# Optimization experiments

Hardware: AMD Instinct MI355X
Metric: run time of the kernel (lower is better)

Reference implementation:

```python
import jax, jax.numpy as jnp
import numpy as np


def ste_round(x):
    # straight-through rounding (identity gradient), as used in brevitas fake-quant
    return x + jax.lax.stop_gradient(jnp.round(x) - x)


def quant_weight(w, bits):
    # symmetric per-tensor int quantization: scale = max|w| / (2^(b-1)-1)
    qmax = 2.0 ** (bits - 1) - 1.0
    s = jnp.max(jnp.abs(w)) / qmax
    return jnp.clip(ste_round(w / s), -qmax, qmax) * s


def quant_relu(x, scale, bits):
    # unsigned act quant (QuantReLU): clip to [0, scale], round to 2^b-1 levels
    n = 2.0 ** bits - 1.0
    step = scale / n
    return ste_round(jnp.clip(x, 0.0, scale) / step) * step


def conv2d(x, w, b, pad):
    # NCHW 'same' conv, stride 1
    y = jax.lax.conv_general_dilated(
        x, w, window_strides=(1, 1),
        padding=[(pad, pad), (pad, pad)],
        dimension_numbers=('NCHW', 'OIHW', 'NCHW'))
    return y + b[None, :, None, None]


def setup_inputs() -> dict:
    key = jax.random.key(0)
    ks = jax.random.split(key, 8)
    B, H, W = 8, 512, 512
    x = jax.random.uniform(ks[0], (B, 1, H, W), dtype=jnp.float32)
    # xavier-ish init scales: gain / sqrt(fan_in + fan_out per kernel elem)
    w1 = jax.random.normal(ks[1], (64, 1, 9, 9), dtype=jnp.float32) * 0.12
    b1 = jax.random.normal(ks[2], (64,), dtype=jnp.float32) * 0.01
    w2 = jax.random.normal(ks[3], (32, 64, 5, 5), dtype=jnp.float32) * 0.03
    b2 = jax.random.normal(ks[4], (32,), dtype=jnp.float32) * 0.01
    w3 = jax.random.normal(ks[5], (1, 32, 5, 5), dtype=jnp.float32) * 0.05
    b3 = jax.random.normal(ks[6], (1,), dtype=jnp.float32) * 0.01
    # activation quant scales (learned params in brevitas; fixed here)
    s1 = jnp.ones((1,), dtype=jnp.float32) * 4.0
    s2 = jnp.ones((1,), dtype=jnp.float32) * 4.0
    s3 = jnp.ones((1,), dtype=jnp.float32) * 2.0
    return {"x": x, "w1": w1, "b1": b1, "w2": w2, "b2": b2,
            "w3": w3, "b3": b3, "s1": s1, "s2": s2, "s3": s3}


def reference(x, w1, b1, w2, b2, w3, b3, s1, s2, s3):
    NBK, NBA, NLACT = 8, 8, 8
    # conv1: 1->64, k=9, pad=4, int8 weights; quant-ReLU (nba bits)
    h = conv2d(x, quant_weight(w1, NBK), b1, pad=4)
    h = quant_relu(h, s1[0], NBA)
    # conv2: 64->32, k=5, pad=2
    h = conv2d(h, quant_weight(w2, NBK), b2, pad=2)
    h = quant_relu(h, s2[0], NBA)
    # conv3: 32->1, k=5, pad=2, last-layer weight bits = nlact = 8
    h = conv2d(h, quant_weight(w3, NLACT), b3, pad=2)
    h = quant_relu(h, s3[0], NLACT)
    return h
```

## Files before the change

kernel.cpp:

```cpp
#include <hip/hip_runtime.h>
#include <cmath>

#define HH 512
#define WW 512
#define BB 8
#define WP (WW + 4)
#define HP (HH + 4)

#define PROWS 520
#define PCOLS 528
#define PT ((size_t)BB * PROWS * PCOLS)

typedef int v4i __attribute__((ext_vector_type(4)));
typedef float v4f __attribute__((ext_vector_type(4)));
typedef _Float16 v8h __attribute__((ext_vector_type(8)));

#if defined(__has_builtin)
#if __has_builtin(__builtin_amdgcn_sdot4)
#define DOT4(a, b, c) __builtin_amdgcn_sdot4((a), (b), (c), false)
#endif
#endif
#ifndef DOT4
static __device__ __forceinline__ int dot4_fb(int a, int b, int c) {
  c += ((a << 24) >> 24) * ((b << 24) >> 24);
  c += ((a << 16) >> 24) * ((b << 16) >> 24);
  c += ((a << 8) >> 24) * ((b << 8) >> 24);
  c += (a >> 24) * (b >> 24);
  return c;
}
#define DOT4(a, b, c) dot4_fb((a), (b), (c))
#endif

static constexpr size_t SCALES_OFF = 0;
static constexpr size_t CORRF_OFF  = 64;
static constexpr size_t FS3_OFF    = 512;
static constexpr size_t QW1_OFF    = 1024;
static constexpr size_t W1FRAG_OFF = 24576;
static constexpr size_t W2S_OFF    = 65536;
static constexpr size_t W3P_OFF    = 131072;
static constexpr size_t H1_OFF     = (size_t)1 << 20;
static constexpr size_t H1_SZ      = (size_t)BB * HP * WP * 64;
static constexpr size_t H2_OFF     = H1_OFF + H1_SZ;
static constexpr size_t H2_SZ      = (size_t)BB * HP * WP * 32;
static constexpr size_t WS_NEED    = H2_OFF + H2_SZ;

__global__ void quant_weights_k(const float* __restrict__ w1,
                                const float* __restrict__ w2,
                                const float* __restrict__ w3,
                                float* __restrict__ scales,
                                float* __restrict__ qw1,
                                signed char* __restrict__ w2s,
                                signed char* __restrict__ w3p) {
  const int t = blockIdx.x;
  const float* src = (t == 0) ? w1 : (t == 1) ? w2 : w3;
  const int n = (t == 0) ? 64 * 81 : (t == 1) ? 32 * 64 * 25 : 32 * 25;
  __shared__ float red[256];
  float m = 0.0f;
  for (int i = threadIdx.x; i < n; i += 256) m = fmaxf(m, fabsf(src[i]));
  red[threadIdx.x] = m;
  __syncthreads();
  for (int s = 128; s > 0; s >>= 1) {
    if ((int)threadIdx.x < s) red[threadIdx.x] = fmaxf(red[threadIdx.x], red[threadIdx.x + s]);
    __syncthreads();
  }
  const float scale = red[0] / 127.0f;
  if (threadIdx.x == 0) scales[t] = scale;
  for (int i = threadIdx.x; i < n; i += 256) {
    float q = rintf(src[i] / scale);
    q = fminf(fmaxf(q, -127.0f), 127.0f);
    if (t == 0) {
      qw1[i] = q;
    } else if (t == 1) {
      const int oc = i / 1600;
      const int r = i - oc * 1600;
      const int ic = r / 25, tap = r - ic * 25;
      w2s[(((tap * 4 + (ic >> 4)) * 32) + oc) * 16 + (ic & 15)] = (signed char)(int)q;
    } else {
      const int ic = i / 25, tap = i - ic * 25;
      w3p[tap * 32 + ic] = (signed char)(int)q;
    }
  }
}

__global__ void prep_k(const signed char* __restrict__ w2s,
                       const signed char* __restrict__ w3p,
                       const float* __restrict__ qw1,
                       int* __restrict__ corrf, int* __restrict__ fs3,
                       unsigned short* __restrict__ w1frag) {
  const int tid = threadIdx.x;
  __shared__ int red3[32];
  {
    const int oc = tid >> 3, part = tid & 7;
    const unsigned int* wd = (const unsigned int*)w2s;
    int s = 0;
    for (int chunk = part; chunk < 100; chunk += 8) {
      const int tap = chunk >> 2, kb = chunk & 3;
      const int base = tap * 512 + kb * 128 + oc * 4;
      #pragma unroll
      for (int j = 0; j < 4; ++j) s = DOT4((int)wd[base + j], 0x01010101, s);
    }
    s += __shfl_xor(s, 1);
    s += __shfl_xor(s, 2);
    s += __shfl_xor(s, 4);
    if (part == 0) corrf[oc] = s;
  }
  if (tid < 32) {
    int s = 0;
    if (tid < 25) {
      const unsigned int* wd = (const unsigned int*)w3p;
      #pragma unroll
      for (int j = 0; j < 8; ++j) s = DOT4((int)wd[tid * 8 + j], 0x01010101, s);
    }
    red3[tid] = s;
  }
  __syncthreads();
  if (tid == 0) {
    int s = 0;
    #pragma unroll
    for (int j = 0; j < 32; ++j) s += red3[j];
    fs3[0] = s;
  }
  for (int i = tid; i < 18432; i += 256) {
    const int e = i & 7, lidx = (i >> 3) & 63, nn = (i >> 9) & 3, j = i >> 11;
    const int t = j * 32 + (lidx >> 4) * 8 + e;
    const int term = (t >= 144) ? 1 : 0;
    const int rem = t - term * 144;
    const int ky = rem >> 4, kx = rem & 15;
    const int oc = nn * 16 + (lidx & 15);
    float v = 0.0f;
    if (kx < 9) v = qw1[oc * 81 + ky * 9 + kx];
    if (term) v *= (1.0f / 4096.0f);
    const _Float16 hv = (_Float16)v;
    w1frag[i] = __builtin_bit_cast(unsigned short, hv);
  }
}

__global__ __launch_bounds__(256) void prep_x_k(const float* __restrict__ x,
                                                unsigned short* __restrict__ planes) {
  const size_t i = (size_t)blockIdx.x * 256 + threadIdx.x;
  if (i >= PT) return;
  const int col = (int)(i % PCOLS);
  const size_t t = i / PCOLS;
  const int row = (int)(t % PROWS);
  const int b = (int)(t / PROWS);
  const float* xb = x + (size_t)b * HH * WW;
  const int xr = row - 4;
  float v0 = 0.0f, v1 = 0.0f;
  if (xr >= 0 && xr < HH) {
    const int c0 = col - 4, c1 = col - 3;
    if (c0 >= 0 && c0 < WW) v0 = xb[(size_t)xr * WW + c0];
    if (c1 >= 0 && c1 < WW) v1 = xb[(size_t)xr * WW + c1];
  }
  const _Float16 h0 = (_Float16)v0;
  const _Float16 l0 = (_Float16)((v0 - (float)h0) * 4096.0f);
  const _Float16 h1 = (_Float16)v1;
  const _Float16 l1 = (_Float16)((v1 - (float)h1) * 4096.0f);
  planes[i]          = __builtin_bit_cast(unsigned short, h0);
  planes[PT + i]     = __builtin_bit_cast(unsigned short, l0);
  planes[2 * PT + i] = __builtin_bit_cast(unsigned short, h1);
  planes[3 * PT + i] = __builtin_bit_cast(unsigned short, l1);
}

__global__ void fill_k(unsigned char* __restrict__ h1p, unsigned char* __restrict__ h2p) {
  const int idx = blockIdx.x * 256 + threadIdx.x;
  const uint4 v = make_uint4(0x80808080u, 0x80808080u, 0x80808080u, 0x80808080u);
  if (idx < 66048) {
    const int q = idx & 3; const int u = idx >> 2;
    const int pxi = u % WP; const int rr = u / WP;
    const int bb = rr >> 2, sel = rr & 3;
    const int row = (sel < 2) ? sel : 512 + sel;
    *(uint4*)(h1p + (((size_t)bb * HP + row) * WP + pxi) * 64 + q * 16) = v;
  } else if (idx < 131584) {
    const int e = idx - 66048; const int q = e & 3; int u = e >> 2;
    const int c = u & 3; u >>= 2;
    const int row = 2 + (u & 511); const int bb = u >> 9;
    const int col = (c < 2) ? c : 512 + c;
    *(uint4*)(h1p + (((size_t)bb * HP + row) * WP + col) * 64 + q * 16) = v;
  } else if (idx < 164608) {
    const int e = idx - 131584; const int q = e & 1; const int u = e >> 1;
    const int pxi = u % WP; const int rr = u / WP;
    const int bb = rr >> 2, sel = rr & 3;
    const int row = (sel < 2) ? sel : 512 + sel;
    *(uint4*)(h2p + (((size_t)bb * HP + row) * WP + pxi) * 32 + q * 16) = v;
  } else {
    const int e = idx - 164608; const int q = e & 1; int u = e >> 1;
    const int c = u & 3; u >>= 2;
    const int row = 2 + (u & 511); const int bb = u >> 9;
    const int col = (c < 2) ? c : 512 + c;
    *(uint4*)(h2p + (((size_t)bb * HP + row) * WP + col) * 32 + q * 16) = v;
  }
}

__global__ __launch_bounds__(512) void conv1_k(
    const unsigned short* __restrict__ planes,
    const unsigned short* __restrict__ w1frag,
    const float* __restrict__ b1,
    const float* __restrict__ scales,
    const float* __restrict__ s1,
    unsigned char* __restrict__ h1p) {
  __shared__ alignas(16) unsigned short wf[18432];
  for (int i = threadIdx.x; i < 2304; i += 512)
    ((int4*)wf)[i] = ((const int4*)w1frag)[i];
  __syncthreads();

  const int y = blockIdx.x & (HH - 1);
  const int b = blockIdx.x >> 9;
  const int l = threadIdx.x & 63;
  const int wv = threadIdx.x >> 6;
  const int pxw = wv * 64;
  const int r = l & 15, kb = l >> 4;

  const unsigned short* pb = planes + (size_t)(r & 1) * (2 * PT)
                           + ((size_t)b * PROWS + y) * PCOLS + (pxw + (r & ~1));
  int offs[9];
  #pragma unroll
  for (int j = 0; j < 9; ++j) {
    const int t0 = j * 32 + kb * 8;
    const int term = (t0 >= 144) ? 1 : 0;
    const int rem = t0 - term * 144;
    offs[j] = term * (int)PT + (rem >> 4) * PCOLS + (rem & 8);
  }

  v4f acc[4][4];
  #pragma unroll
  for (int p = 0; p < 4; ++p)
    #pragma unroll
    for (int o = 0; o < 4; ++o) acc[p][o] = (v4f){0.f, 0.f, 0.f, 0.f};

  #pragma unroll
  for (int j = 0; j < 9; ++j) {
    v8h av[4];
    #pragma unroll
    for (int p = 0; p < 4; ++p) {
      const void* ap = __builtin_assume_aligned((const void*)(pb + offs[j] + p * 16), 4);
      uint4 tv;
      __builtin_memcpy(&tv, ap, 16);
      av[p] = __builtin_bit_cast(v8h, tv);
    }
    #pragma unroll
    for (int o = 0; o < 4; ++o) {
      const v8h bw = *(const v8h*)(wf + ((size_t)(j * 4 + o) * 64 + l) * 8);
      #pragma unroll
      for (int p = 0; p < 4; ++p)
        acc[p][o] = __builtin_amdgcn_mfma_f32_16x16x32_f16(bw, av[p], acc[p][o], 0, 0, 0);
    }
  }

  const float ws1 = scales[0];
  const float sc = s1[0], step = sc / 255.0f;
  unsigned int* ob = (unsigned int*)(h1p
      + (((size_t)b * HP + y + 2) * WP + 2 + pxw + r) * 64 + kb * 4);
  #pragma unroll
  for (int o = 0; o < 4; ++o) {
    const v4f bv = *(const v4f*)(b1 + o * 16 + kb * 4);
    #pragma unroll
    for (int p = 0; p < 4; ++p) {
      unsigned int dw = 0;
      #pragma unroll
      for (int reg = 0; reg < 4; ++reg) {
        const float h = acc[p][o][reg] * ws1 + bv[reg];
        const float c = fminf(fmaxf(h, 0.0f), sc);
        int qi = (int)rintf(c / step);
        qi = qi < 0 ? 0 : (qi > 255 ? 255 : qi);
        dw |= (unsigned int)(qi ^ 0x80) << (8 * reg);
      }
      ob[p * 256 + o * 4] = dw;
    }
  }
}

__global__ __launch_bounds__(256) void conv2_k(
    const unsigned char* __restrict__ h1p,
    const signed char* __restrict__ w2g,
    const int* __restrict__ corrf,
    const float* __restrict__ b2,
    const float* __restrict__ scales,
    const float* __restrict__ s1, const float* __restrict__ s2,
    unsigned char* __restrict__ h2p) {
  const int l = threadIdx.x & 63;
  const int wv = threadIdx.x >> 6;
  const int r = l & 15, kb = l >> 4;
  const int y = blockIdx.y * 4;
  const int b = blockIdx.z;
  const int xw = blockIdx.x * 64 + wv * 16;

  v4i acc[4][2];
  #pragma unroll
  for (int t = 0; t < 4; ++t)
    #pragma unroll
    for (int n = 0; n < 2; ++n) acc[t][n] = (v4i){0, 0, 0, 0};

  const size_t rstride = (size_t)WP * 64;
  const unsigned char* abase = h1p + (((size_t)b * HP + y) * WP + xw + r) * 64 + kb * 16;
  const signed char* wl = w2g + kb * 512 + r * 16;

  v4i a_cur[8], a_nxt[8];
  #pragma unroll
  for (int j = 0; j < 8; ++j) a_cur[j] = *(const v4i*)(abase + j * rstride);

  #pragma unroll
  for (int kx = 0; kx < 5; ++kx) {
    if (kx < 4) {
      #pragma unroll
      for (int j = 0; j < 8; ++j)
        a_nxt[j] = *(const v4i*)(abase + (kx + 1) * 64 + j * rstride);
    }
    #pragma unroll
    for (int ky = 0; ky < 5; ++ky) {
      const signed char* wt = wl + (ky * 5 + kx) * 2048;
      const v4i bf0 = *(const v4i*)(wt);
      const v4i bf1 = *(const v4i*)(wt + 256);
      #pragma unroll
      for (int t = 0; t < 4; ++t) {
        acc[t][0] = __builtin_amdgcn_mfma_i32_16x16x64_i8(bf0, a_cur[ky + t], acc[t][0], 0, 0, 0);
        acc[t][1] = __builtin_amdgcn_mfma_i32_16x16x64_i8(bf1, a_cur[ky + t], acc[t][1], 0, 0, 0);
      }
    }
    if (kx < 4) {
      #pragma unroll
      for (int j = 0; j < 8; ++j) a_cur[j] = a_nxt[j];
    }
  }

  const float step1 = s1[0] / 255.0f;
  const float sc2 = s2[0], step2 = sc2 / 255.0f;
  const float asc = step1 * scales[1];
  #pragma unroll
  for (int n = 0; n < 2; ++n) {
    const v4f bv = *(const v4f*)(b2 + n * 16 + kb * 4);
    const v4i cv = *(const v4i*)(corrf + n * 16 + kb * 4);
    #pragma unroll
    for (int t = 0; t < 4; ++t) {
      unsigned int* ob = (unsigned int*)(h2p
          + (((size_t)b * HP + y + t + 2) * WP + xw + 2 + r) * 32 + n * 16 + kb * 4);
      unsigned int dw = 0;
      #pragma unroll
      for (int reg = 0; reg < 4; ++reg) {
        const float v = (float)(acc[t][n][reg] + cv[reg] * 128) * asc + bv[reg];
        const float c = fminf(fmaxf(v, 0.0f), sc2);
        int qi = (int)rintf(c / step2);
        qi = qi < 0 ? 0 : (qi > 255 ? 255 : qi);
        dw |= (unsigned int)(qi ^ 0x80) << (8 * reg);
      }
      *ob = dw;
    }
  }
}

__global__ __launch_bounds__(256) void conv3_k(
    const unsigned char* __restrict__ h2p,
    const signed char* __restrict__ w3p,
    const int* __restrict__ fs3,
    const float* __restrict__ b3,
    const float* __restrict__ scales,
    const float* __restrict__ s2, const float* __restrict__ s3,
    float* __restrict__ out) {
  const int p  = blockIdx.x * 256 + threadIdx.x;
  const int px = p & (WW - 1);
  const int py = (p >> 9) & (HH - 1);
  const int bz = p >> 18;

  const int* wq = (const int*)w3p;
  const unsigned char* base = h2p + (((size_t)bz * HP + py) * WP + px) * 32;

  int acc = 0;
  #pragma unroll
  for (int ky = 0; ky < 5; ++ky) {
    const v4i* rp = (const v4i*)(base + (size_t)ky * WP * 32);
    v4i c[10];
    #pragma unroll
    for (int g = 0; g < 10; ++g) c[g] = rp[g];
    const int* wrow = wq + ky * 40;
    #pragma unroll
    for (int kx = 0; kx < 5; ++kx) {
      #pragma unroll
      for (int g = 0; g < 8; ++g) {
        const int idx = kx * 8 + g;
        acc = DOT4(c[idx >> 2][idx & 3], wrow[idx], acc);
      }
    }
  }

  const int tot = acc + fs3[0] * 128;
  const float step2 = s2[0] / 255.0f;
  const float sc3 = s3[0], step3 = sc3 / 255.0f;
  const float y = (float)tot * (step2 * scales[2]) + b3[0];
  const float c = fminf(fmaxf(y, 0.0f), sc3);
  float q = rintf(c / step3);
  q = fminf(fmaxf(q, 0.0f), 255.0f);
  out[p] = q * step3;
}

extern "C" void kernel_launch(void* const* d_in, const int* in_sizes, int n_in,
                              void* d_out, int out_size, void* d_ws, size_t ws_size,
                              hipStream_t stream) {
  const float* x  = (const float*)d_in[0];
  const float* w1 = (const float*)d_in[1];
  const float* b1 = (const float*)d_in[2];
  const float* w2 = (const float*)d_in[3];
  const float* b2 = (const float*)d_in[4];
  const float* w3 = (const float*)d_in[5];
  const float* b3 = (const float*)d_in[6];
  const float* s1 = (const float*)d_in[7];
  const float* s2 = (const float*)d_in[8];
  const float* s3 = (const float*)d_in[9];

  if (ws_size < WS_NEED) return;

  char* ws = (char*)d_ws;
  float*          scales  = (float*)(ws + SCALES_OFF);
  int*            corrf   = (int*)(ws + CORRF_OFF);
  int*            fs3     = (int*)(ws + FS3_OFF);
  float*          qw1     = (float*)(ws + QW1_OFF);
  unsigned short* w1frag  = (unsigned short*)(ws + W1FRAG_OFF);
  signed char*    w2s     = (signed char*)(ws + W2S_OFF);
  signed char*    w3p     = (signed char*)(ws + W3P_OFF);
  unsigned char*  h1p     = (unsigned char*)(ws + H1_OFF);
  unsigned char*  h2p     = (unsigned char*)(ws + H2_OFF);
  unsigned short* planes  = (unsigned short*)(ws + H2_OFF);

  quant_weights_k<<<3, 256, 0, stream>>>(w1, w2, w3, scales, qw1, w2s, w3p);
  prep_k<<<1, 256, 0, stream>>>(w2s, w3p, qw1, corrf, fs3, w1frag);
  prep_x_k<<<(int)(PT / 256), 256, 0, stream>>>(x, planes);

  conv1_k<<<BB * HH, 512, 0, stream>>>(planes, w1frag, b1, scales, s1, h1p);
  fill_k<<<771, 256, 0, stream>>>(h1p, h2p);

  dim3 g2(8, 128, BB);
  conv2_k<<<g2, 256, 0, stream>>>(h1p, w2s, corrf, b2, scales, s1, s2, h2p);

  const int npix = BB * HH * WW;
  conv3_k<<<npix / 256, 256, 0, stream>>>(h2p, w3p, fs3, b3, scales, s2, s3, (float*)d_out);
}
```

Measured before the change: 487.0 us.

## Switch conv2 to 32x32x32 int8 MFMA with LDS-staged weights

Rewrites conv2 to use the 32x32x32 int8 MFMA, so each wave covers 32 pixels by all 32 output channels instead of issuing paired 16x16x64 ops. The full 50KB quantized weight tensor is copied into shared memory per block and read from there, and the weight layout in the quantization and correction-sum kernels is changed to match the new fragment order. The grid now gives each wave its own 4-row strip. This should improve MFMA efficiency and cut global weight reads, at the cost of a per-block weight copy and high LDS use that may limit occupancy. The old register prefetch of the next kx activations is also dropped.

Result: faster. 440.7 us (-9.5%).

```diff
diff --git a/kernel.cpp b/kernel.cpp
--- a/kernel.cpp
+++ b/kernel.cpp
@@ -12,6 +12,7 @@
 #define PT ((size_t)BB * PROWS * PCOLS)
 
 typedef int v4i __attribute__((ext_vector_type(4)));
+typedef int v16i __attribute__((ext_vector_type(16)));
 typedef float v4f __attribute__((ext_vector_type(4)));
 typedef _Float16 v8h __attribute__((ext_vector_type(8)));
 
@@ -74,7 +75,9 @@
       const int oc = i / 1600;
       const int r = i - oc * 1600;
       const int ic = r / 25, tap = r - ic * 25;
-      w2s[(((tap * 4 + (ic >> 4)) * 32) + oc) * 16 + (ic & 15)] = (signed char)(int)q;
+      const int addr = (tap * 2 + (ic >> 5)) * 1024 + ((ic >> 4) & 1) * 512
+                     + oc * 16 + (ic & 15);
+      w2s[addr] = (signed char)(int)q;
     } else {
       const int ic = i / 25, tap = i - ic * 25;
       w3p[tap * 32 + ic] = (signed char)(int)q;
@@ -94,8 +97,7 @@
     const unsigned int* wd = (const unsigned int*)w2s;
     int s = 0;
     for (int chunk = part; chunk < 100; chunk += 8) {
-      const int tap = chunk >> 2, kb = chunk & 3;
-      const int base = tap * 512 + kb * 128 + oc * 4;
+      const int base = chunk * 128 + oc * 4;
       #pragma unroll
       for (int j = 0; j < 4; ++j) s = DOT4((int)wd[base + j], 0x01010101, s);
     }
@@ -271,54 +273,56 @@
 
 __global__ __launch_bounds__(256) void conv2_k(
     const unsigned char* __restrict__ h1p,
-    const signed char* __restrict__ w2g,
+    const int4* __restrict__ w2s,
     const int* __restrict__ corrf,
     const float* __restrict__ b2,
     const float* __restrict__ scales,
     const float* __restrict__ s1, const float* __restrict__ s2,
     unsigned char* __restrict__ h2p) {
+  __shared__ alignas(16) signed char wlds[51200];
+  __shared__ alignas(16) int clds[32];
+  {
+    int4* dst = (int4*)wlds;
+    for (int i = threadIdx.x; i < 3200; i += 256) dst[i] = w2s[i];
+    if (threadIdx.x < 32) clds[threadIdx.x] = corrf[threadIdx.x];
+  }
+  __syncthreads();
+
   const int l = threadIdx.x & 63;
   const int wv = threadIdx.x >> 6;
-  const int r = l & 15, kb = l >> 4;
-  const int y = blockIdx.y * 4;
+  const int pl = l & 31;
+  const int hi = l >> 5;
+  const int y = blockIdx.y * 16 + wv * 4;
   const int b = blockIdx.z;
-  const int xw = blockIdx.x * 64 + wv * 16;
-
-  v4i acc[4][2];
+  const int xw = blockIdx.x * 32;
+
+  v16i acc[4];
   #pragma unroll
   for (int t = 0; t < 4; ++t)
     #pragma unroll
-    for (int n = 0; n < 2; ++n) acc[t][n] = (v4i){0, 0, 0, 0};
+    for (int e = 0; e < 16; ++e) acc[t][e] = 0;
 
   const size_t rstride = (size_t)WP * 64;
-  const unsigned char* abase = h1p + (((size_t)b * HP + y) * WP + xw + r) * 64 + kb * 16;
-  const signed char* wl = w2g + kb * 512 + r * 16;
-
-  v4i a_cur[8], a_nxt[8];
-  #pragma unroll
-  for (int j = 0; j < 8; ++j) a_cur[j] = *(const v4i*)(abase + j * rstride);
+  const unsigned char* abase = h1p + (((size_t)b * HP + y) * WP + xw + pl) * 64 + hi * 16;
+  const signed char* wbase = wlds + l * 16;
 
   #pragma unroll
   for (int kx = 0; kx < 5; ++kx) {
-    if (kx < 4) {
-      #pragma unroll
-      for (int j = 0; j < 8; ++j)
-        a_nxt[j] = *(const v4i*)(abase + (kx + 1) * 64 + j * rstride);
+    v4i a[8][2];
+    #pragma unroll
+    for (int row = 0; row < 8; ++row) {
+      a[row][0] = *(const v4i*)(abase + kx * 64 + row * rstride);
+      a[row][1] = *(const v4i*)(abase + kx * 64 + row * rstride + 32);
     }
     #pragma unroll
     for (int ky = 0; ky < 5; ++ky) {
-      const signed char* wt = wl + (ky * 5 + kx) * 2048;
-      const v4i bf0 = *(const v4i*)(wt);
-      const v4i bf1 = *(const v4i*)(wt + 256);
-      #pragma unroll
-      for (int t = 0; t < 4; ++t) {
-        acc[t][0] = __builtin_amdgcn_mfma_i32_16x16x64_i8(bf0, a_cur[ky + t], acc[t][0], 0, 0, 0);
-        acc[t][1] = __builtin_amdgcn_mfma_i32_16x16x64_i8(bf1, a_cur[ky + t], acc[t][1], 0, 0, 0);
+      #pragma unroll
+      for (int h = 0; h < 2; ++h) {
+        const v4i wfr = *(const v4i*)(wbase + ((ky * 5 + kx) * 2 + h) * 1024);
+        #pragma unroll
+        for (int t = 0; t < 4; ++t)
+          acc[t] = __builtin_amdgcn_mfma_i32_32x32x32_i8(wfr, a[ky + t][h], acc[t], 0, 0, 0);
       }
-    }
-    if (kx < 4) {
-      #pragma unroll
-      for (int j = 0; j < 8; ++j) a_cur[j] = a_nxt[j];
     }
   }
 
@@ -326,23 +330,23 @@
   const float sc2 = s2[0], step2 = sc2 / 255.0f;
   const float asc = step1 * scales[1];
   #pragma unroll
-  for (int n = 0; n < 2; ++n) {
-    const v4f bv = *(const v4f*)(b2 + n * 16 + kb * 4);
-    const v4i cv = *(const v4i*)(corrf + n * 16 + kb * 4);
-    #pragma unroll
-    for (int t = 0; t < 4; ++t) {
-      unsigned int* ob = (unsigned int*)(h2p
-          + (((size_t)b * HP + y + t + 2) * WP + xw + 2 + r) * 32 + n * 16 + kb * 4);
+  for (int t = 0; t < 4; ++t) {
+    unsigned char* ob = h2p + (((size_t)b * HP + y + t + 2) * WP + xw + 2 + pl) * 32 + hi * 4;
+    #pragma unroll
+    for (int g = 0; g < 4; ++g) {
+      const int ocb = g * 8 + hi * 4;
+      const v4f bv = *(const v4f*)(b2 + ocb);
+      const v4i cv = *(const v4i*)(clds + ocb);
       unsigned int dw = 0;
       #pragma unroll
-      for (int reg = 0; reg < 4; ++reg) {
-        const float v = (float)(acc[t][n][reg] + cv[reg] * 128) * asc + bv[reg];
+      for (int q = 0; q < 4; ++q) {
+        const float v = (float)(acc[t][g * 4 + q] + cv[q] * 128) * asc + bv[q];
         const float c = fminf(fmaxf(v, 0.0f), sc2);
         int qi = (int)rintf(c / step2);
         qi = qi < 0 ? 0 : (qi > 255 ? 255 : qi);
-        dw |= (unsigned int)(qi ^ 0x80) << (8 * reg);
+        dw |= (unsigned int)(qi ^ 0x80) << (8 * q);
       }
-      *ob = dw;
+      *(unsigned int*)(ob + g * 8) = dw;
     }
   }
 }
@@ -426,8 +430,8 @@
   conv1_k<<<BB * HH, 512, 0, stream>>>(planes, w1frag, b1, scales, s1, h1p);
   fill_k<<<771, 256, 0, stream>>>(h1p, h2p);
 
-  dim3 g2(8, 128, BB);
-  conv2_k<<<g2, 256, 0, stream>>>(h1p, w2s, corrf, b2, scales, s1, s2, h2p);
+  dim3 g2(16, 32, BB);
+  conv2_k<<<g2, 256, 0, stream>>>(h1p, (const int4*)w2s, corrf, b2, scales, s1, s2, h2p);
 
   const int npix = BB * HH * WW;
   conv3_k<<<npix / 256, 256, 0, stream>>>(h2p, w3p, fs3, b3, scales, s2, s3, (float*)d_out);
```
